# Performance work log

Hardware: AMD Instinct MI355X
Metric: run time of the kernel (lower is better)

Reference implementation:

```python
import jax, jax.numpy as jnp
import numpy as np

B, S, H = 1, 2048, 4096
NH, NKV, HD = 32, 8, 128
GROUPS = NH // NKV  # 4
THETA = 10000.0
NEG = -1e9


def setup_inputs() -> dict:
    key = jax.random.key(0)
    k1, k2, k3 = jax.random.split(key, 3)
    hidden_states = jax.random.normal(k1, (B, S, H), dtype=jnp.float32)
    w_qkv = jax.random.normal(k2, (H, (NH + 2 * NKV) * HD), dtype=jnp.float32) * 0.02
    w_o = jax.random.normal(k3, (NH * HD, H), dtype=jnp.float32) * 0.02
    causal = jnp.tril(jnp.ones((S, S), dtype=bool))
    attention_mask = jnp.where(causal, 0.0, NEG).astype(jnp.float32)[None, None]  # [1,1,S,S]
    return {"hidden_states": hidden_states, "w_qkv": w_qkv, "w_o": w_o,
            "attention_mask": attention_mask}


def _rope_freqs(seqlen, head_dim, theta):
    inv = 1.0 / (theta ** (jnp.arange(0, head_dim, 2, dtype=jnp.float32) / head_dim))
    t = jnp.arange(seqlen, dtype=jnp.float32)
    freqs = t[:, None] * inv[None, :]              # [S, HD/2]
    return jnp.cos(freqs), jnp.sin(freqs)


def _apply_rope(x, cos, sin):
    # x: [B,S,heads,HD]; source pairs x[i] with x[i+HD/2] (NeoX rotate-half)
    half = x.shape[-1] // 2
    x1, x2 = x[..., :half], x[..., half:]
    c = cos[None, :, None, :]
    s = sin[None, :, None, :]
    return jnp.concatenate([x1 * c - x2 * s, x1 * s + x2 * c], axis=-1)


def reference(hidden_states, w_qkv, w_o, attention_mask):
    bsz, seqlen, _ = hidden_states.shape
    xqkv = hidden_states @ w_qkv                            # [B,S,(NH+2*NKV)*HD]
    xqkv = xqkv.reshape(bsz, seqlen, NH + 2 * NKV, HD)
    xq = xqkv[:, :, :NH]                                    # [B,S,NH,HD]
    xk = xqkv[:, :, NH:NH + NKV]                            # [B,S,NKV,HD]
    xv = xqkv[:, :, NH + NKV:]                              # [B,S,NKV,HD]

    cos, sin = _rope_freqs(seqlen, HD, THETA)               # start_pos = 0 (prefill)
    xq = _apply_rope(xq, cos, sin)
    xk = _apply_rope(xk, cos, sin)

    # GQA: repeat kv heads to match query heads
    keys = jnp.repeat(xk, GROUPS, axis=2)                   # [B,S,NH,HD]
    values = jnp.repeat(xv, GROUPS, axis=2)

    scores = jnp.einsum('bqhd,bkhd->bhqk', xq, keys) / np.sqrt(HD)
    scores = scores + attention_mask
    probs = jax.nn.softmax(scores.astype(jnp.float32), axis=-1).astype(xq.dtype)
    out = jnp.einsum('bhqk,bkhd->bqhd', probs, values)      # [B,S,NH,HD]
    attention_weight = out.reshape(bsz, seqlen, NH * HD)
    attn_output = attention_weight @ w_o                    # [B,S,H]
    return attn_output
```

## Files before the change

kernel.cpp:

```cpp
#include <hip/hip_runtime.h>

typedef __bf16 bf16_8 __attribute__((ext_vector_type(8)));
typedef float f32x4 __attribute__((ext_vector_type(4)));
typedef unsigned short ushort8v __attribute__((ext_vector_type(8)));
typedef unsigned short ushort4v __attribute__((ext_vector_type(4)));

#define SEQ 2048
#define HDIM 4096
#define NHEADS 32
#define NKVH 8
#define HEADD 128
#define NQKV 6144

__device__ __forceinline__ unsigned short f2bf(float f) {
    unsigned int u = __float_as_uint(f);
    u += 0x7fffu + ((u >> 16) & 1u);
    return (unsigned short)(u >> 16);
}
__device__ __forceinline__ float bf2f(unsigned short v) {
    return __uint_as_float(((unsigned int)v) << 16);
}

#if defined(__has_builtin)
#if __has_builtin(__builtin_amdgcn_exp2f)
#define EXP2(x) __builtin_amdgcn_exp2f(x)
#endif
#endif
#ifndef EXP2
#define EXP2(x) __expf(0.69314718055994531f * (x))
#endif

typedef __attribute__((address_space(1))) void as1_void;
typedef __attribute__((address_space(3))) void as3_void;
__device__ __forceinline__ void gload16(const unsigned short* g, unsigned short* l) {
    __builtin_amdgcn_global_load_lds((as1_void*)g, (as3_void*)l, 16, 0, 0);
}

__global__ void k_f32_to_bf16(const float* __restrict__ in, unsigned short* __restrict__ out, int n) {
    int i = (blockIdx.x * blockDim.x + threadIdx.x) * 4;
    if (i >= n) return;
    float4 v = *reinterpret_cast<const float4*>(in + i);
    ushort4v o = { f2bf(v.x), f2bf(v.y), f2bf(v.z), f2bf(v.w) };
    *reinterpret_cast<ushort4v*>(out + i) = o;
}

__global__ void k_transpose_f32_to_bf16(const float* __restrict__ in, unsigned short* __restrict__ out,
                                        int K, int N) {
    __shared__ unsigned short tile[64][72];
    int k0 = blockIdx.y * 64, n0 = blockIdx.x * 64;
    int t = threadIdx.x;
    int r = t >> 2;
    int cs = (t & 3) * 16;
    int sw = (r >> 4) * 16;
    const float* src = in + (size_t)(k0 + r) * N + n0 + cs;
#pragma unroll
    for (int j = 0; j < 16; j += 4) {
        float4 v = *reinterpret_cast<const float4*>(src + j);
        tile[r][(cs + j + 0) ^ sw] = f2bf(v.x);
        tile[r][(cs + j + 1) ^ sw] = f2bf(v.y);
        tile[r][(cs + j + 2) ^ sw] = f2bf(v.z);
        tile[r][(cs + j + 3) ^ sw] = f2bf(v.w);
    }
    __syncthreads();
    int rr = t >> 2;
    int ks = (t & 3) * 16;
    unsigned short tmp[16];
#pragma unroll
    for (int i = 0; i < 16; i++) tmp[i] = tile[ks + i][rr ^ (((ks + i) >> 4) * 16)];
    unsigned short* dst = out + (size_t)(n0 + rr) * K + k0 + ks;
    *reinterpret_cast<ushort8v*>(dst) = *reinterpret_cast<const ushort8v*>(tmp);
    *reinterpret_cast<ushort8v*>(dst + 8) = *reinterpret_cast<const ushort8v*>(tmp + 8);
}

__global__ void k_transpose_bf16(const unsigned short* __restrict__ in, unsigned short* __restrict__ out,
                                 int inStride, int outStride) {
    __shared__ unsigned short tile[64][72];
    int r0 = blockIdx.y * 64, c0 = blockIdx.x * 64;
    int t = threadIdx.x;
    int r = t >> 2;
    int cs = (t & 3) * 16;
    int csw = cs ^ ((r >> 4) * 16);
    const unsigned short* src = in + (size_t)(r0 + r) * inStride + c0 + cs;
    *reinterpret_cast<ushort8v*>(&tile[r][csw])     = *reinterpret_cast<const ushort8v*>(src);
    *reinterpret_cast<ushort8v*>(&tile[r][csw + 8]) = *reinterpret_cast<const ushort8v*>(src + 8);
    __syncthreads();
    int rr = t >> 2;
    int ks = (t & 3) * 16;
    unsigned short tmp[16];
#pragma unroll
    for (int i = 0; i < 16; i++) tmp[i] = tile[ks + i][rr ^ (((ks + i) >> 4) * 16)];
    unsigned short* dst = out + (size_t)(c0 + rr) * outStride + r0 + ks;
    *reinterpret_cast<ushort8v*>(dst) = *reinterpret_cast<const ushort8v*>(tmp);
    *reinterpret_cast<ushort8v*>(dst + 8) = *reinterpret_cast<const ushort8v*>(tmp + 8);
}


#define RG(BUF, KH) (smem + ((BUF) * 2 + (KH)) * PR)

#define STAGE_A(TILE, KH) do { if ((TILE) < NT) {                                        \
    size_t kb_ = (size_t)(TILE) * 128 + (size_t)((KH) * 64);                             \
    char* d_ = RG((TILE) & 1, KH) + wby;                                                 \
    gload16((const unsigned short*)(srcA0 + kb_), (unsigned short*)d_);                  \
    gload16((const unsigned short*)(srcA1 + kb_), (unsigned short*)(d_ + 8192));         \
  } } while (0)

#define STAGE_B(TILE, KH) do { if ((TILE) < NT) {                                        \
    size_t kb_ = (size_t)(TILE) * 128 + (size_t)((KH) * 64);                             \
    char* d_ = RG((TILE) & 1, KH) + 16384 + wby;                                         \
    gload16((const unsigned short*)(srcB0 + kb_), (unsigned short*)d_);                  \
    if constexpr (BN == 256)                                                             \
        gload16((const unsigned short*)(srcB1 + kb_), (unsigned short*)(d_ + 8192));     \
  } } while (0)

#define VMW_N() do {                                                                     \
    if constexpr (BN == 256) asm volatile("s_waitcnt vmcnt(8)" ::: "memory");            \
    else                     asm volatile("s_waitcnt vmcnt(6)" ::: "memory");            \
  } while (0)

#define TAILVM() do {                                                                    \
    if (tail) asm volatile("s_waitcnt vmcnt(0)" ::: "memory");                           \
    else      VMW_N();                                                                   \
  } while (0)

#define PHASE(PB, PKH, PMH, STAGE_STMT, VM_STMT) do {                                    \
    const char* ab_ = RG(PB, PKH);                                                       \
    bf16_8 av_[MF2];                                                                     \
    _Pragma("unroll")                                                                    \
    for (int mi_ = 0; mi_ < MF2; ++mi_)                                                  \
        av_[mi_] = *(const bf16_8*)(ab_ + offA[(PMH) * MF2 + mi_]);                      \
    if ((PMH) == 0) {                                                                    \
        _Pragma("unroll")                                                                \
        for (int nj_ = 0; nj_ < 4; ++nj_)                                                \
            bv[nj_] = *(const bf16_8*)(ab_ + 16384 + offB[nj_]);                         \
    }                                                                                    \
    STAGE_STMT;                                                                          \
    VM_STMT;                                                                             \
    __builtin_amdgcn_s_barrier();                                                        \
    __builtin_amdgcn_s_setprio(1);                                                       \
    _Pragma("unroll")                                                                    \
    for (int mi_ = 0; mi_ < MF2; ++mi_) {                                                \
        _Pragma("unroll")                                                                \
        for (int nj_ = 0; nj_ < 4; ++nj_)                                                \
            acc[(PMH) * MF2 + mi_][nj_] = __builtin_amdgcn_mfma_f32_16x16x32_bf16(       \
                av_[mi_], bv[nj_], acc[(PMH) * MF2 + mi_][nj_], 0, 0, 0);                \
    }                                                                                    \
    __builtin_amdgcn_s_setprio(0);                                                       \
    asm volatile("s_waitcnt lgkmcnt(0)" ::: "memory");                                   \
    __builtin_amdgcn_s_barrier();                                                        \
  } while (0)

template <int BN, int WM, int WN, bool OUT_BF16, bool FUSE_T>
__global__ __launch_bounds__(512, 2) void k_gemm256(
    const unsigned short* __restrict__ A,
    const unsigned short* __restrict__ Bt,
    void* __restrict__ Cv,
    int N, int K, int nwgemm, int ntn,
    const float* __restrict__ TPin, unsigned short* __restrict__ TPout)
{
    extern __shared__ char smem[];
    constexpr int PWR = 256 / WM;
    constexpr int PWC = BN / WN;
    constexpr int MF  = PWR / 16;
    constexpr int MF2 = MF / 2;
    constexpr int PR  = 16384 + BN * 64;
    int t = threadIdx.x;

    if constexpr (FUSE_T) {
        if ((int)blockIdx.x >= nwgemm) {
            int tb = blockIdx.x - nwgemm;
            int half = t >> 8, lt = t & 255;
            unsigned short* tile = (unsigned short*)smem + half * (64 * 72);
            int r = lt >> 2, cs = (lt & 3) * 16, sw = (r >> 4) * 16;
            for (int i = 0; i < 32; ++i) {
                int tau = tb * 64 + i * 2 + half;
                int n0 = (tau & 63) * 64, k0 = (tau >> 6) * 64;
                const float* src = TPin + (size_t)(k0 + r) * 4096 + n0 + cs;
#pragma unroll
                for (int j = 0; j < 16; j += 4) {
                    float4 v = *reinterpret_cast<const float4*>(src + j);
                    tile[r * 72 + ((cs + j + 0) ^ sw)] = f2bf(v.x);
                    tile[r * 72 + ((cs + j + 1) ^ sw)] = f2bf(v.y);
                    tile[r * 72 + ((cs + j + 2) ^ sw)] = f2bf(v.z);
                    tile[r * 72 + ((cs + j + 3) ^ sw)] = f2bf(v.w);
                }
                __syncthreads();
                unsigned short tmp[16];
#pragma unroll
                for (int q = 0; q < 16; q++)
                    tmp[q] = tile[(cs + q) * 72 + (r ^ (((cs + q) >> 4) * 16))];
                unsigned short* dst = TPout + (size_t)(n0 + r) * 4096 + k0 + cs;
                *reinterpret_cast<ushort8v*>(dst) = *reinterpret_cast<const ushort8v*>(tmp);
                *reinterpret_cast<ushort8v*>(dst + 8) = *reinterpret_cast<const ushort8v*>(tmp + 8);
                __syncthreads();
            }
            return;
        }
    }

    const int NT = K >> 6;
    int bid = blockIdx.x;
    int cpx = nwgemm >> 3;
    int sw_ = (bid & 7) * cpx + (bid >> 3);
    int tm = sw_ / ntn, tn = sw_ % ntn;
    int gm0 = tm << 8, gn0 = tn * BN;

    int w = t >> 6, lane = t & 63;
    int l15 = lane & 15, quad = lane >> 4;
    int wr = w / WN, wc = w % WN;
    int wby = w << 10;

    int offA[MF], offB[4];
#pragma unroll
    for (int mh = 0; mh < 2; mh++)
#pragma unroll
        for (int mi = 0; mi < MF2; mi++) {
            int row = wr * PWR + mh * (PWR / 2) + mi * 16 + l15;
            offA[mh * MF2 + mi] = row * 64 + ((quad ^ ((row >> 1) & 3)) << 4);
        }
#pragma unroll
    for (int nj = 0; nj < 4; nj++) {
        int row = wc * PWC + nj * 16 + l15;
        offB[nj] = row * 64 + ((quad ^ ((row >> 1) & 3)) << 4);
    }

    int srow0 = t >> 2;
    int sslot = (t & 3) ^ ((srow0 >> 1) & 3);
    const char* srcA0 = (const char*)A  + ((size_t)(gm0 + srow0)       * K + sslot * 8) * 2;
    const char* srcA1 = (const char*)A  + ((size_t)(gm0 + srow0 + 128) * K + sslot * 8) * 2;
    const char* srcB0 = (const char*)Bt + ((size_t)(gn0 + srow0)       * K + sslot * 8) * 2;
    const char* srcB1 = (BN == 256)
        ? (const char*)Bt + ((size_t)(gn0 + srow0 + 128) * K + sslot * 8) * 2
        : srcB0;

    f32x4 acc[MF][4] = {};
    bf16_8 bv[4];

    STAGE_A(0, 0); STAGE_B(0, 0);
    STAGE_A(0, 1); STAGE_B(0, 1);
    STAGE_A(1, 0); STAGE_B(1, 0);
    VMW_N();
    __builtin_amdgcn_s_barrier();

    const int NITER = K >> 7;
    for (int it = 0; it < NITER; ++it) {
        int T1 = 2 * it + 1, T2 = T1 + 1, T3 = T1 + 2;
        bool tail = (it == NITER - 1);
        PHASE(0, 0, 0, STAGE_A(T1, 1), ((void)0));
        PHASE(0, 0, 1, STAGE_B(T1, 1), VMW_N());
        PHASE(0, 1, 0, STAGE_A(T2, 0), ((void)0));
        PHASE(0, 1, 1, STAGE_B(T2, 0), TAILVM());
        PHASE(1, 0, 0, STAGE_A(T2, 1), ((void)0));
        PHASE(1, 0, 1, STAGE_B(T2, 1), VMW_N());
        PHASE(1, 1, 0, STAGE_A(T3, 0), ((void)0));
        PHASE(1, 1, 1, STAGE_B(T3, 0), VMW_N());
    }

    int crow = gm0 + wr * PWR + quad * 4;
    int ccol = gn0 + wc * PWC + l15;
#pragma unroll
    for (int m = 0; m < MF; m++)
#pragma unroll
        for (int nj = 0; nj < 4; nj++)
#pragma unroll
            for (int r = 0; r < 4; r++) {
                size_t idx = (size_t)(crow + m * 16 + r) * N + (ccol + nj * 16);
                float v = acc[m][nj][r];
                if (OUT_BF16) ((unsigned short*)Cv)[idx] = f2bf(v);
                else          ((float*)Cv)[idx] = v;
            }
}

#undef RG
#undef STAGE_A
#undef STAGE_B
#undef VMW_N
#undef TAILVM
#undef PHASE

__global__ void k_rope_split(const unsigned short* __restrict__ qkv,
                             unsigned short* __restrict__ Qb,
                             unsigned short* __restrict__ Kb)
{
    int wid = blockIdx.x * 4 + (threadIdx.x >> 6);
    int lane = threadIdx.x & 63;
    int head = wid % 40;
    int s = wid / 40;
    const unsigned short* src = qkv + (size_t)s * NQKV + head * HEADD;
    float x1 = bf2f(src[lane]);
    float x2 = bf2f(src[lane + 64]);
    float inv = __expf(-(float)lane * 0.14391156831212787f);
    float ang = (float)s * inv;
    float sn, c;
    __sincosf(ang, &sn, &c);
    float o1 = x1 * c - x2 * sn;
    float o2 = x1 * sn + x2 * c;
    unsigned short* dst;
    if (head < 32) {
        const float s2 = 0.12752908270648427f;
        o1 *= s2; o2 *= s2;
        dst = Qb + ((size_t)head * SEQ + s) * HEADD;
    } else {
        dst = Kb + ((size_t)(head - 32) * SEQ + s) * HEADD;
    }
    dst[lane] = f2bf(o1);
    dst[lane + 64] = f2bf(o2);
}

__global__ __launch_bounds__(256, 4) void k_attention(
    const unsigned short* __restrict__ Qb,
    const unsigned short* __restrict__ Kb,
    const unsigned short* __restrict__ Vt,
    unsigned short* __restrict__ Ob)
{
    __shared__ unsigned short Ks[64][136];
    __shared__ unsigned short Vs[128][72];
    __shared__ unsigned short Ps[4][16][72];
    int h  = blockIdx.y;
    int hkv = h >> 2;
    int t = threadIdx.x;
    int w = t >> 6, lane = t & 63, l15 = lane & 15, quad = lane >> 4;

    const unsigned short* kbase = Kb + (size_t)hkv * SEQ * HEADD;
    const unsigned short* vbase = Vt + (size_t)hkv * HEADD * SEQ;

    int qtile[2] = { (int)blockIdx.x, 31 - (int)blockIdx.x };

    for (int ph = 0; ph < 2; ph++) {
        int q0 = qtile[ph] * 64;
        int qm0 = q0 + w * 16;
        int qg = qm0 + l15;

        bf16_8 aq[4];
        {
            const unsigned short* qp = Qb + ((size_t)h * SEQ + qg) * HEADD + quad * 8;
#pragma unroll
            for (int kk = 0; kk < 4; kk++)
                aq[kk] = *reinterpret_cast<const bf16_8*>(qp + kk * 32);
        }

        f32x4 o[8] = {};
        float l_ = 0.f;

        for (int kv0 = 0; kv0 < q0 + 64; kv0 += 64) {
            __syncthreads();
#pragma unroll
            for (int p = 0; p < 4; p++) {
                int r = p * 16 + (t >> 4), c = (t & 15) * 8;
                *reinterpret_cast<ushort8v*>(&Ks[r][c]) =
                    *reinterpret_cast<const ushort8v*>(kbase + (size_t)(kv0 + r) * HEADD + c);
            }
#pragma unroll
            for (int p = 0; p < 4; p++) {
                int r = p * 32 + (t >> 3), c = (t & 7) * 8;
                *reinterpret_cast<ushort8v*>(&Vs[r][c]) =
                    *reinterpret_cast<const ushort8v*>(vbase + (size_t)r * SEQ + kv0 + c);
            }
            __syncthreads();

            if (kv0 > qm0 + 15) continue;

            f32x4 sc[4];
#pragma unroll
            for (int nt = 0; nt < 4; nt++) {
                f32x4 z = {};
#pragma unroll
                for (int kk = 0; kk < 4; kk++) {
                    bf16_8 bk = *reinterpret_cast<const bf16_8*>(&Ks[nt * 16 + l15][kk * 32 + quad * 8]);
                    z = __builtin_amdgcn_mfma_f32_16x16x32_bf16(bk, aq[kk], z, 0, 0, 0);
                }
                sc[nt] = z;
            }
            bool needMask = (kv0 + 63 > qm0);
#pragma unroll
            for (int nt = 0; nt < 4; nt++)
#pragma unroll
                for (int r = 0; r < 4; r++) {
                    float a = sc[nt][r] - 12.0f;
                    if (needMask) {
                        int kg = kv0 + nt * 16 + quad * 4 + r;
                        if (kg > qg) a = -1000.0f;
                    }
                    float p = EXP2(a);
                    sc[nt][r] = p;
                    l_ += p;
                }
#pragma unroll
            for (int nt = 0; nt < 4; nt++) {
                ushort4v pk = { f2bf(sc[nt][0]), f2bf(sc[nt][1]), f2bf(sc[nt][2]), f2bf(sc[nt][3]) };
                *reinterpret_cast<ushort4v*>(&Ps[w][l15][nt * 16 + quad * 4]) = pk;
            }
            asm volatile("s_waitcnt lgkmcnt(0)" ::: "memory");
            bf16_8 pf[2];
#pragma unroll
            for (int kk = 0; kk < 2; kk++)
                pf[kk] = *reinterpret_cast<const bf16_8*>(&Ps[w][l15][kk * 32 + quad * 8]);
#pragma unroll
            for (int dt = 0; dt < 8; dt++)
#pragma unroll
                for (int kk = 0; kk < 2; kk++) {
                    bf16_8 av = *reinterpret_cast<const bf16_8*>(&Vs[dt * 16 + l15][kk * 32 + quad * 8]);
                    o[dt] = __builtin_amdgcn_mfma_f32_16x16x32_bf16(av, pf[kk], o[dt], 0, 0, 0);
                }
        }
        l_ += __shfl_xor(l_, 16, 64);
        l_ += __shfl_xor(l_, 32, 64);
        float rinv = 1.0f / l_;
        unsigned short* orow = Ob + (size_t)qg * (NHEADS * HEADD) + h * HEADD + quad * 4;
#pragma unroll
        for (int dt = 0; dt < 8; dt++) {
            ushort4v pk = { f2bf(o[dt][0] * rinv), f2bf(o[dt][1] * rinv),
                            f2bf(o[dt][2] * rinv), f2bf(o[dt][3] * rinv) };
            *reinterpret_cast<ushort4v*>(orow + dt * 16) = pk;
        }
    }
}

extern "C" void kernel_launch(void* const* d_in, const int* in_sizes, int n_in,
                              void* d_out, int out_size, void* d_ws, size_t ws_size,
                              hipStream_t stream) {
    const float* hs    = (const float*)d_in[0];
    const float* w_qkv = (const float*)d_in[1];
    const float* w_o   = (const float*)d_in[2];

    static bool s_attr_set = false;
    if (!s_attr_set) {
        hipFuncSetAttribute(reinterpret_cast<const void*>(k_gemm256<256, 2, 4, true, true>),
                            hipFuncAttributeMaxDynamicSharedMemorySize, 131072);
        hipFuncSetAttribute(reinterpret_cast<const void*>(k_gemm256<128, 4, 2, false, false>),
                            hipFuncAttributeMaxDynamicSharedMemorySize, 131072);
        s_attr_set = true;
    }

    char* ws = (char*)d_ws;
    size_t off = 0;
    auto alloc = [&](size_t bytes) -> void* {
        void* p = ws + off;
        off += (bytes + 255) & ~(size_t)255;
        return p;
    };
    unsigned short* Xb    = (unsigned short*)alloc((size_t)SEQ * HDIM * 2);
    unsigned short* R1    = (unsigned short*)alloc((size_t)NQKV * HDIM * 2);
    unsigned short* Wot   = (unsigned short*)alloc((size_t)HDIM * HDIM * 2);
    unsigned short* QKVb  = (unsigned short*)alloc((size_t)SEQ * NQKV * 2);
    unsigned short* Wqkvt = R1;
    unsigned short* Qb = R1;
    unsigned short* Kb = Qb + (size_t)NHEADS * SEQ * HEADD;
    unsigned short* Vt = Kb + (size_t)NKVH * SEQ * HEADD;
    unsigned short* AOb = Xb;

    k_f32_to_bf16<<<(SEQ * HDIM) / 1024, 256, 0, stream>>>(hs, Xb, SEQ * HDIM);
    k_transpose_f32_to_bf16<<<dim3(NQKV / 64, HDIM / 64), 256, 0, stream>>>(w_qkv, Wqkvt, HDIM, NQKV);
    k_gemm256<256, 2, 4, true, true><<<dim3(256), dim3(512), 131072, stream>>>(
        Xb, Wqkvt, QKVb, NQKV, HDIM, 192, NQKV / 256, w_o, Wot);
    k_rope_split<<<(SEQ * 40) / 4, 256, 0, stream>>>(QKVb, Qb, Kb);
    k_transpose_bf16<<<dim3((NKVH * HEADD) / 64, SEQ / 64), 256, 0, stream>>>(
        QKVb + (size_t)(NHEADS + NKVH) * HEADD, Vt, NQKV, SEQ);
    k_attention<<<dim3(16, NHEADS), 256, 0, stream>>>(Qb, Kb, Vt, AOb);
    k_gemm256<128, 4, 2, false, false><<<dim3(256), dim3(512), 98304, stream>>>(
        AOb, Wot, d_out, HDIM, HDIM, 256, HDIM / 128, nullptr, nullptr);
}
```

Measured before the change: 486.0 us.

## Pipeline attention K/V loads with async double-buffered LDS and restage output GEMM

The attention kernel moves to 512-thread blocks over 128-row query tiles, paired so each block handles one early and one late tile. K/V tiles are prefetched with direct global-to-LDS loads into swizzled double buffers, replacing synchronous register-staged copies and their two syncthreads per tile. The BN=128 output GEMM now stages A and B together per phase, with one full-M compute phase per K half instead of two half-M phases. This aims to hide load latency and halve barrier count, at the cost of more LDS per block and possibly lower occupancy.

```diff
diff --git a/kernel.cpp b/kernel.cpp
--- a/kernel.cpp
+++ b/kernel.cpp
@@ -112,6 +112,8 @@
         gload16((const unsigned short*)(srcB1 + kb_), (unsigned short*)(d_ + 8192));     \
   } } while (0)
 
+#define STAGE_AB(TILE, KH) do { STAGE_A(TILE, KH); STAGE_B(TILE, KH); } while (0)
+
 #define VMW_N() do {                                                                     \
     if constexpr (BN == 256) asm volatile("s_waitcnt vmcnt(8)" ::: "memory");            \
     else                     asm volatile("s_waitcnt vmcnt(6)" ::: "memory");            \
@@ -122,13 +124,18 @@
     else      VMW_N();                                                                   \
   } while (0)
 
-#define PHASE(PB, PKH, PMH, STAGE_STMT, VM_STMT) do {                                    \
+#define VM_T(NT_, TL_) do {                                                              \
+    if (tail) asm volatile("s_waitcnt vmcnt(" #TL_ ")" ::: "memory");                    \
+    else      asm volatile("s_waitcnt vmcnt(" #NT_ ")" ::: "memory");                    \
+  } while (0)
+
+#define PHASE_G(PB, PKH, MBASE, MCNT, DOB, STAGE_STMT, VM_STMT) do {                     \
     const char* ab_ = RG(PB, PKH);                                                       \
-    bf16_8 av_[MF2];                                                                     \
+    bf16_8 av_[MCNT];                                                                    \
     _Pragma("unroll")                                                                    \
-    for (int mi_ = 0; mi_ < MF2; ++mi_)                                                  \
-        av_[mi_] = *(const bf16_8*)(ab_ + offA[(PMH) * MF2 + mi_]);                      \
-    if ((PMH) == 0) {                                                                    \
+    for (int mi_ = 0; mi_ < (MCNT); ++mi_)                                               \
+        av_[mi_] = *(const bf16_8*)(ab_ + offA[(MBASE) + mi_]);                          \
+    if (DOB) {                                                                           \
         _Pragma("unroll")                                                                \
         for (int nj_ = 0; nj_ < 4; ++nj_)                                                \
             bv[nj_] = *(const bf16_8*)(ab_ + 16384 + offB[nj_]);                         \
@@ -138,11 +145,11 @@
     __builtin_amdgcn_s_barrier();                                                        \
     __builtin_amdgcn_s_setprio(1);                                                       \
     _Pragma("unroll")                                                                    \
-    for (int mi_ = 0; mi_ < MF2; ++mi_) {                                                \
+    for (int mi_ = 0; mi_ < (MCNT); ++mi_) {                                             \
         _Pragma("unroll")                                                                \
         for (int nj_ = 0; nj_ < 4; ++nj_)                                                \
-            acc[(PMH) * MF2 + mi_][nj_] = __builtin_amdgcn_mfma_f32_16x16x32_bf16(       \
-                av_[mi_], bv[nj_], acc[(PMH) * MF2 + mi_][nj_], 0, 0, 0);                \
+            acc[(MBASE) + mi_][nj_] = __builtin_amdgcn_mfma_f32_16x16x32_bf16(           \
+                av_[mi_], bv[nj_], acc[(MBASE) + mi_][nj_], 0, 0, 0);                    \
     }                                                                                    \
     __builtin_amdgcn_s_setprio(0);                                                       \
     asm volatile("s_waitcnt lgkmcnt(0)" ::: "memory");                                   \
@@ -235,24 +242,39 @@
     f32x4 acc[MF][4] = {};
     bf16_8 bv[4];
 
-    STAGE_A(0, 0); STAGE_B(0, 0);
-    STAGE_A(0, 1); STAGE_B(0, 1);
-    STAGE_A(1, 0); STAGE_B(1, 0);
-    VMW_N();
-    __builtin_amdgcn_s_barrier();
-
     const int NITER = K >> 7;
-    for (int it = 0; it < NITER; ++it) {
-        int T1 = 2 * it + 1, T2 = T1 + 1, T3 = T1 + 2;
-        bool tail = (it == NITER - 1);
-        PHASE(0, 0, 0, STAGE_A(T1, 1), ((void)0));
-        PHASE(0, 0, 1, STAGE_B(T1, 1), VMW_N());
-        PHASE(0, 1, 0, STAGE_A(T2, 0), ((void)0));
-        PHASE(0, 1, 1, STAGE_B(T2, 0), TAILVM());
-        PHASE(1, 0, 0, STAGE_A(T2, 1), ((void)0));
-        PHASE(1, 0, 1, STAGE_B(T2, 1), VMW_N());
-        PHASE(1, 1, 0, STAGE_A(T3, 0), ((void)0));
-        PHASE(1, 1, 1, STAGE_B(T3, 0), VMW_N());
+
+    if constexpr (BN == 256) {
+        STAGE_A(0, 0); STAGE_B(0, 0);
+        STAGE_A(0, 1); STAGE_B(0, 1);
+        STAGE_A(1, 0); STAGE_B(1, 0);
+        VMW_N();
+        __builtin_amdgcn_s_barrier();
+        for (int it = 0; it < NITER; ++it) {
+            int T1 = 2 * it + 1, T2 = T1 + 1, T3 = T1 + 2;
+            bool tail = (it == NITER - 1);
+            PHASE_G(0, 0, 0,   MF2, 1, STAGE_A(T1, 1), ((void)0));
+            PHASE_G(0, 0, MF2, MF2, 0, STAGE_B(T1, 1), VMW_N());
+            PHASE_G(0, 1, 0,   MF2, 1, STAGE_A(T2, 0), ((void)0));
+            PHASE_G(0, 1, MF2, MF2, 0, STAGE_B(T2, 0), TAILVM());
+            PHASE_G(1, 0, 0,   MF2, 1, STAGE_A(T2, 1), ((void)0));
+            PHASE_G(1, 0, MF2, MF2, 0, STAGE_B(T2, 1), VMW_N());
+            PHASE_G(1, 1, 0,   MF2, 1, STAGE_A(T3, 0), ((void)0));
+            PHASE_G(1, 1, MF2, MF2, 0, STAGE_B(T3, 0), VMW_N());
+        }
+    } else {
+        STAGE_AB(0, 0); STAGE_AB(0, 1); STAGE_AB(1, 0);
+        asm volatile("s_waitcnt vmcnt(6)" ::: "memory");
+        __builtin_amdgcn_s_barrier();
+        for (int it = 0; it < NITER; ++it) {
+            int T1 = 2 * it + 1, T2 = T1 + 1, T3 = T1 + 2;
+            bool tail = (it == NITER - 1);
+            PHASE_G(0, 0, 0, MF, 1, STAGE_AB(T1, 1),
+                    asm volatile("s_waitcnt vmcnt(6)" ::: "memory"));
+            PHASE_G(0, 1, 0, MF, 1, STAGE_AB(T2, 0), VM_T(6, 3));
+            PHASE_G(1, 0, 0, MF, 1, STAGE_AB(T2, 1), VM_T(6, 0));
+            PHASE_G(1, 1, 0, MF, 1, STAGE_AB(T3, 0), VM_T(6, 0));
+        }
     }
 
     int crow = gm0 + wr * PWR + quad * 4;
@@ -273,9 +295,11 @@
 #undef RG
 #undef STAGE_A
 #undef STAGE_B
+#undef STAGE_AB
 #undef VMW_N
 #undef TAILVM
-#undef PHASE
+#undef VM_T
+#undef PHASE_G
 
 __global__ void k_rope_split(const unsigned short* __restrict__ qkv,
                              unsigned short* __restrict__ Qb,
@@ -306,66 +330,111 @@
     dst[lane + 64] = f2bf(o2);
 }
 
-__global__ __launch_bounds__(256, 4) void k_attention(
+__global__ __launch_bounds__(512, 2) void k_attention(
     const unsigned short* __restrict__ Qb,
     const unsigned short* __restrict__ Kb,
     const unsigned short* __restrict__ Vt,
     unsigned short* __restrict__ Ob)
 {
-    __shared__ unsigned short Ks[64][136];
-    __shared__ unsigned short Vs[128][72];
-    __shared__ unsigned short Ps[4][16][72];
-    int h  = blockIdx.y;
-    int hkv = h >> 2;
+    extern __shared__ char smem[];
+    unsigned short* Ps = (unsigned short*)(smem + 65536);
+    int h = blockIdx.y, hkv = h >> 2;
+    int b = blockIdx.x;
     int t = threadIdx.x;
     int w = t >> 6, lane = t & 63, l15 = lane & 15, quad = lane >> 4;
-
-    const unsigned short* kbase = Kb + (size_t)hkv * SEQ * HEADD;
-    const unsigned short* vbase = Vt + (size_t)hkv * HEADD * SEQ;
-
-    int qtile[2] = { (int)blockIdx.x, 31 - (int)blockIdx.x };
-
-    for (int ph = 0; ph < 2; ph++) {
-        int q0 = qtile[ph] * 64;
-        int qm0 = q0 + w * 16;
-        int qg = qm0 + l15;
-
-        bf16_8 aq[4];
-        {
-            const unsigned short* qp = Qb + ((size_t)h * SEQ + qg) * HEADD + quad * 8;
-#pragma unroll
-            for (int kk = 0; kk < 4; kk++)
-                aq[kk] = *reinterpret_cast<const bf16_8*>(qp + kk * 32);
-        }
-
-        f32x4 o[8] = {};
-        float l_ = 0.f;
-
-        for (int kv0 = 0; kv0 < q0 + 64; kv0 += 64) {
-            __syncthreads();
-#pragma unroll
-            for (int p = 0; p < 4; p++) {
-                int r = p * 16 + (t >> 4), c = (t & 15) * 8;
-                *reinterpret_cast<ushort8v*>(&Ks[r][c]) =
-                    *reinterpret_cast<const ushort8v*>(kbase + (size_t)(kv0 + r) * HEADD + c);
+    int x7 = l15 & 7;
+
+    const char* kbase = (const char*)(Kb + (size_t)hkv * SEQ * HEADD);
+    const char* vbase = (const char*)(Vt + (size_t)hkv * HEADD * SEQ);
+
+    int rK0 = w * 4 + (lane >> 4), rK1 = rK0 + 32;
+    size_t SK0 = (size_t)rK0 * 256 + (size_t)(((lane & 15) ^ (rK0 & 7)) << 4);
+    size_t SK1 = (size_t)rK1 * 256 + (size_t)(((lane & 15) ^ (rK1 & 7)) << 4);
+    int rV0 = w * 8 + (lane >> 3), rV1 = rV0 + 64;
+    size_t SV0 = (size_t)rV0 * 4096 + (size_t)(((lane & 7) ^ (rV0 & 7)) << 4);
+    size_t SV1 = (size_t)rV1 * 4096 + (size_t)(((lane & 7) ^ (rV1 & 7)) << 4);
+
+    const int nA = 2 * b + 2;
+    const int NI = 34;
+    int qm0  = b * 128 + w * 16;
+    int qm0B = (15 - b) * 128 + w * 16;
+    int qg  = qm0 + l15;
+    int qgB = qm0B + l15;
+
+    bf16_8 aq[4], aqB[4];
+    {
+        const unsigned short* qpA = Qb + ((size_t)h * SEQ + qg) * HEADD + quad * 8;
+        const unsigned short* qpB = Qb + ((size_t)h * SEQ + qgB) * HEADD + quad * 8;
+#pragma unroll
+        for (int kk = 0; kk < 4; kk++) {
+            aq[kk]  = *reinterpret_cast<const bf16_8*>(qpA + kk * 32);
+            aqB[kk] = *reinterpret_cast<const bf16_8*>(qpB + kk * 32);
+        }
+    }
+
+    f32x4 o[8] = {};
+    float l_ = 0.f;
+
+    {
+        char* dK = smem + w * 1024;
+        gload16((const unsigned short*)(kbase + SK0), (unsigned short*)dK);
+        gload16((const unsigned short*)(kbase + SK1), (unsigned short*)(dK + 8192));
+        char* dV = smem + 16384 + w * 1024;
+        gload16((const unsigned short*)(vbase + SV0), (unsigned short*)dV);
+        gload16((const unsigned short*)(vbase + SV1), (unsigned short*)(dV + 8192));
+    }
+
+    for (int ii = 0; ii < NI; ++ii) {
+        if (ii + 1 < NI) {
+            int j = ii + 1;
+            int kvn = (j < nA ? j : j - nA) << 6;
+            const char* kb = kbase + (size_t)kvn * 256;
+            const char* vb = vbase + (size_t)kvn * 2;
+            char* dK = smem + (j & 1) * 32768 + w * 1024;
+            gload16((const unsigned short*)(kb + SK0), (unsigned short*)dK);
+            gload16((const unsigned short*)(kb + SK1), (unsigned short*)(dK + 8192));
+            char* dV = smem + (j & 1) * 32768 + 16384 + w * 1024;
+            gload16((const unsigned short*)(vb + SV0), (unsigned short*)dV);
+            gload16((const unsigned short*)(vb + SV1), (unsigned short*)(dV + 8192));
+            asm volatile("s_waitcnt vmcnt(4)" ::: "memory");
+        } else {
+            asm volatile("s_waitcnt vmcnt(0)" ::: "memory");
+        }
+        __builtin_amdgcn_s_barrier();
+
+        if (ii == nA) {
+            float lr = l_;
+            lr += __shfl_xor(lr, 16, 64);
+            lr += __shfl_xor(lr, 32, 64);
+            float rinv = 1.0f / lr;
+            unsigned short* orow = Ob + (size_t)qg * (NHEADS * HEADD) + h * HEADD + quad * 4;
+#pragma unroll
+            for (int dt = 0; dt < 8; dt++) {
+                ushort4v pk = { f2bf(o[dt][0] * rinv), f2bf(o[dt][1] * rinv),
+                                f2bf(o[dt][2] * rinv), f2bf(o[dt][3] * rinv) };
+                *reinterpret_cast<ushort4v*>(orow + dt * 16) = pk;
             }
 #pragma unroll
-            for (int p = 0; p < 4; p++) {
-                int r = p * 32 + (t >> 3), c = (t & 7) * 8;
-                *reinterpret_cast<ushort8v*>(&Vs[r][c]) =
-                    *reinterpret_cast<const ushort8v*>(vbase + (size_t)r * SEQ + kv0 + c);
-            }
-            __syncthreads();
-
-            if (kv0 > qm0 + 15) continue;
-
+            for (int kk = 0; kk < 4; kk++) aq[kk] = aqB[kk];
+            qm0 = qm0B; qg = qgB;
+#pragma unroll
+            for (int dt = 0; dt < 8; dt++) o[dt] = (f32x4){0.f, 0.f, 0.f, 0.f};
+            l_ = 0.f;
+        }
+
+        int kv0 = (ii < nA ? ii : ii - nA) << 6;
+        const unsigned short* Kbuf = (const unsigned short*)(smem + (ii & 1) * 32768);
+        const unsigned short* Vbuf = Kbuf + 8192;
+
+        if (kv0 <= qm0 + 15) {
             f32x4 sc[4];
 #pragma unroll
             for (int nt = 0; nt < 4; nt++) {
                 f32x4 z = {};
 #pragma unroll
                 for (int kk = 0; kk < 4; kk++) {
-                    bf16_8 bk = *reinterpret_cast<const bf16_8*>(&Ks[nt * 16 + l15][kk * 32 + quad * 8]);
+                    bf16_8 bk = *reinterpret_cast<const bf16_8*>(
+                        &Kbuf[(nt * 16 + l15) * 128 + (((kk * 4 + quad) ^ x7) << 3)]);
                     z = __builtin_amdgcn_mfma_f32_16x16x32_bf16(bk, aq[kk], z, 0, 0, 0);
                 }
                 sc[nt] = z;
@@ -384,34 +453,39 @@
                     sc[nt][r] = p;
                     l_ += p;
                 }
+            unsigned short* prow = Ps + (w * 16 + l15) * 72;
 #pragma unroll
             for (int nt = 0; nt < 4; nt++) {
                 ushort4v pk = { f2bf(sc[nt][0]), f2bf(sc[nt][1]), f2bf(sc[nt][2]), f2bf(sc[nt][3]) };
-                *reinterpret_cast<ushort4v*>(&Ps[w][l15][nt * 16 + quad * 4]) = pk;
+                *reinterpret_cast<ushort4v*>(prow + nt * 16 + quad * 4) = pk;
             }
             asm volatile("s_waitcnt lgkmcnt(0)" ::: "memory");
             bf16_8 pf[2];
 #pragma unroll
             for (int kk = 0; kk < 2; kk++)
-                pf[kk] = *reinterpret_cast<const bf16_8*>(&Ps[w][l15][kk * 32 + quad * 8]);
+                pf[kk] = *reinterpret_cast<const bf16_8*>(prow + kk * 32 + quad * 8);
 #pragma unroll
             for (int dt = 0; dt < 8; dt++)
 #pragma unroll
                 for (int kk = 0; kk < 2; kk++) {
-                    bf16_8 av = *reinterpret_cast<const bf16_8*>(&Vs[dt * 16 + l15][kk * 32 + quad * 8]);
+                    bf16_8 av = *reinterpret_cast<const bf16_8*>(
+                        &Vbuf[(dt * 16 + l15) * 64 + (((kk * 4 + quad) ^ x7) << 3)]);
                     o[dt] = __builtin_amdgcn_mfma_f32_16x16x32_bf16(av, pf[kk], o[dt], 0, 0, 0);
                 }
         }
-        l_ += __shfl_xor(l_, 16, 64);
-        l_ += __shfl_xor(l_, 32, 64);
-        float rinv = 1.0f / l_;
-        unsigned short* orow = Ob + (size_t)qg * (NHEADS * HEADD) + h * HEADD + quad * 4;
-#pragma unroll
-        for (int dt = 0; dt < 8; dt++) {
-            ushort4v pk = { f2bf(o[dt][0] * rinv), f2bf(o[dt][1] * rinv),
-                            f2bf(o[dt][2] * rinv), f2bf(o[dt][3] * rinv) };
-            *reinterpret_cast<ushort4v*>(orow + dt * 16) = pk;
-        }
+        asm volatile("s_waitcnt lgkmcnt(0)" ::: "memory");
+        __builtin_amdgcn_s_barrier();
+    }
+
+    l_ += __shfl_xor(l_, 16, 64);
+    l_ += __shfl_xor(l_, 32, 64);
+    float rinv = 1.0f / l_;
+    unsigned short* orow = Ob + (size_t)qg * (NHEADS * HEADD) + h * HEADD + quad * 4;
+#pragma unroll
+    for (int dt = 0; dt < 8; dt++) {
+        ushort4v pk = { f2bf(o[dt][0] * rinv), f2bf(o[dt][1] * rinv),
+                        f2bf(o[dt][2] * rinv), f2bf(o[dt][3] * rinv) };
+        *reinterpret_cast<ushort4v*>(orow + dt * 16) = pk;
     }
 }
 
@@ -427,6 +501,8 @@
         hipFuncSetAttribute(reinterpret_cast<const void*>(k_gemm256<256, 2, 4, true, true>),
                             hipFuncAttributeMaxDynamicSharedMemorySize, 131072);
         hipFuncSetAttribute(reinterpret_cast<const void*>(k_gemm256<128, 4, 2, false, false>),
+                            hipFuncAttributeMaxDynamicSharedMemorySize, 131072);
+        hipFuncSetAttribute(reinterpret_cast<const void*>(k_attention),
                             hipFuncAttributeMaxDynamicSharedMemorySize, 131072);
         s_attr_set = true;
     }
@@ -455,7 +531,7 @@
     k_rope_split<<<(SEQ * 40) / 4, 256, 0, stream>>>(QKVb, Qb, Kb);
     k_transpose_bf16<<<dim3((NKVH * HEADD) / 64, SEQ / 64), 256, 0, stream>>>(
         QKVb + (size_t)(NHEADS + NKVH) * HEADD, Vt, NQKV, SEQ);
-    k_attention<<<dim3(16, NHEADS), 256, 0, stream>>>(Qb, Kb, Vt, AOb);
+    k_attention<<<dim3(8, NHEADS), dim3(512), 83968, stream>>>(Qb, Kb, Vt, AOb);
     k_gemm256<128, 4, 2, false, false><<<dim3(256), dim3(512), 98304, stream>>>(
         AOb, Wot, d_out, HDIM, HDIM, 256, HDIM / 128, nullptr, nullptr);
 }
```

Result: faster. 474.4 us (-2.4%).
